# Optimization experiments

Measured on AMD Instinct MI355X. Metric: run time of the kernel, lower is better.

Reference implementation:

```python
import jax, jax.numpy as jnp
import numpy as np

D_IN = 1024
D_OUT = 1024
N_HEADS = 16
D_H = D_OUT // N_HEADS


def setup_inputs() -> dict:
    key = jax.random.key(0)
    k_x, k_q, k_k, k_v = jax.random.split(key, 4)
    x = jax.random.normal(k_x, (4, 2048, D_IN), dtype=jnp.float32)
    s = 1.0 / np.sqrt(D_IN)
    # weights stored as [d_in, d_out] (transpose of torch Linear.weight)
    W_q = jax.random.uniform(k_q, (D_IN, D_OUT), dtype=jnp.float32, minval=-s, maxval=s)
    W_k = jax.random.uniform(k_k, (D_IN, D_OUT), dtype=jnp.float32, minval=-s, maxval=s)
    W_v = jax.random.uniform(k_v, (D_IN, D_OUT), dtype=jnp.float32, minval=-s, maxval=s)
    return {"x": x, "W_q": W_q, "W_k": W_k, "W_v": W_v}


def reference(x, W_q, W_k, W_v):
    B, T, _ = x.shape
    # QKV projections -> [B, H, T, d_h]
    def split_heads(y):
        return y.reshape(B, T, N_HEADS, D_H).transpose(0, 2, 1, 3)
    q = split_heads(x @ W_q)
    k = split_heads(x @ W_k)
    v = split_heads(x @ W_v)
    # attention scores [B, H, T, T]
    scores = jnp.einsum('bhqd,bhkd->bhqk', q, k)
    causal = jnp.tril(jnp.ones((T, T), dtype=bool))  # True = keep
    scores = jnp.where(causal, scores, -jnp.inf)
    weights = jax.nn.softmax(scores / np.sqrt(D_H), axis=-1)
    ctx = jnp.einsum('bhqk,bhkd->bhqd', weights, v)  # [B,H,T,d_h]
    return ctx.transpose(0, 2, 1, 3).reshape(B, T, D_OUT)
```

## Files before the change

### kernel.cpp

```cpp
#include <hip/hip_runtime.h>
#include <stdint.h>

typedef float f32x4 __attribute__((ext_vector_type(4)));
typedef __bf16 bf16x8 __attribute__((ext_vector_type(8)));

#define LOG2E 1.4426950408889634f
#define SCL2 (0.125f * LOG2E)

static __device__ __forceinline__ unsigned short f2bf(float f) {
  unsigned int u = __builtin_bit_cast(unsigned int, f);
  u += 0x7fffu + ((u >> 16) & 1u);
  return (unsigned short)(u >> 16);
}

static __device__ __forceinline__ void gload16(const void* g, void* l) {
  __builtin_amdgcn_global_load_lds(
      (const __attribute__((address_space(1))) unsigned int*)g,
      (__attribute__((address_space(3))) unsigned int*)l, 16, 0, 0);
}

__global__ void cvt_x_kernel(const float* __restrict__ x, unsigned short* __restrict__ xb) {
  size_t i = ((size_t)blockIdx.x * 256 + threadIdx.x) * 8;
  const float4 a = *(const float4*)(x + i);
  const float4 b = *(const float4*)(x + i + 4);
  union { unsigned short us[8]; uint4 u; } o;
  o.us[0] = f2bf(a.x); o.us[1] = f2bf(a.y); o.us[2] = f2bf(a.z); o.us[3] = f2bf(a.w);
  o.us[4] = f2bf(b.x); o.us[5] = f2bf(b.y); o.us[6] = f2bf(b.z); o.us[7] = f2bf(b.w);
  *(uint4*)(xb + i) = o.u;
}

__global__ void wt_kernel(const float* __restrict__ Wq, const float* __restrict__ Wk,
                          const float* __restrict__ Wv, unsigned short* __restrict__ Wt) {
  __shared__ float t[32][33];
  const int z = blockIdx.z;
  const float* W = (z == 0) ? Wq : ((z == 1) ? Wk : Wv);
  unsigned short* o = Wt + (size_t)z * 1048576;
  const int k0 = blockIdx.y * 32, n0 = blockIdx.x * 32;
  const int tx = threadIdx.x, ty = threadIdx.y;
#pragma unroll
  for (int i = 0; i < 4; ++i)
    t[ty + i * 8][tx] = W[(size_t)(k0 + ty + i * 8) * 1024 + n0 + tx];
  __syncthreads();
#pragma unroll
  for (int i = 0; i < 4; ++i)
    o[(size_t)(n0 + ty + i * 8) * 1024 + k0 + tx] = f2bf(t[tx][ty + i * 8]);
}

__global__ __launch_bounds__(256) void gemm_qkv(
    const unsigned short* __restrict__ xb, const unsigned short* __restrict__ Wt,
    unsigned short* __restrict__ Qb, unsigned short* __restrict__ Kb,
    unsigned short* __restrict__ Vtb) {
  __shared__ uint4 ldsab[2048];
  char* ldsc = (char*)ldsab;
  const int tid = threadIdx.x;
  const int lane = tid & 63;
  const int li = lane & 15, g = lane >> 4;
  const int wv = tid >> 6, wr = wv >> 1, wc = wv & 1;
  const int L = blockIdx.x;
  const int W = (L & 7) * 192 + (L >> 3);
  const int z = W >> 9;
  const int rem = W & 511;
  const int m0 = (rem >> 3) * 128, n0 = (rem & 7) * 128;
  const char* Abase = (const char*)xb;
  const char* Bbase = (const char*)(Wt + (size_t)z * 1048576);

  const f32x4 fz = {0.f, 0.f, 0.f, 0.f};
  f32x4 acc[4][4];
#pragma unroll
  for (int m = 0; m < 4; ++m)
#pragma unroll
    for (int n = 0; n < 4; ++n) acc[m][n] = fz;

  for (int kt = 0; kt < 16; ++kt) {
    __syncthreads();
#pragma unroll
    for (int i = 0; i < 4; ++i) {
      const int c = i * 256 + tid, r = c >> 3, cr = c & 7;
      gload16(Abase + (size_t)(m0 + r) * 2048 + kt * 128 + ((cr ^ (r & 7)) * 16),
              ldsc + c * 16);
      gload16(Bbase + (size_t)(n0 + r) * 2048 + kt * 128 + ((cr ^ (r & 7)) * 16),
              ldsc + 16384 + c * 16);
    }
    __syncthreads();
#pragma unroll
    for (int ks = 0; ks < 2; ++ks) {
      bf16x8 a[4], b[4];
#pragma unroll
      for (int m = 0; m < 4; ++m) {
        const int ra = wr * 64 + m * 16 + li;
        a[m] = *(const bf16x8*)(ldsc + ra * 128 + (((ks * 4 + g) ^ (ra & 7)) * 16));
      }
#pragma unroll
      for (int n = 0; n < 4; ++n) {
        const int rb = wc * 64 + n * 16 + li;
        b[n] = *(const bf16x8*)(ldsc + 16384 + rb * 128 + (((ks * 4 + g) ^ (rb & 7)) * 16));
      }
#pragma unroll
      for (int m = 0; m < 4; ++m)
#pragma unroll
        for (int n = 0; n < 4; ++n)
          acc[m][n] = __builtin_amdgcn_mfma_f32_16x16x32_bf16(a[m], b[n], acc[m][n], 0, 0, 0);
    }
  }

  if (z == 2) {
    __syncthreads();
    char* tb = ldsc + wv * 8192;
#pragma unroll
    for (int m = 0; m < 4; ++m)
#pragma unroll
      for (int n = 0; n < 4; ++n) {
        const int d_l = n * 16 + li;
#pragma unroll
        for (int rp = 0; rp < 2; ++rp) {
          const int t_l = m * 16 + g * 4 + rp * 2;
          const unsigned lo = f2bf(acc[m][n][rp * 2]);
          const unsigned hi2 = f2bf(acc[m][n][rp * 2 + 1]);
          *(unsigned*)(tb + d_l * 128 + (((t_l >> 3) ^ (d_l & 7)) * 16) + (t_l & 7) * 2) =
              lo | (hi2 << 16);
        }
      }
    __syncthreads();
    const int t0g = m0 + wr * 64;
    const int bI2 = t0g >> 11, tt2 = t0g & 2047;
    const int hh = (n0 + wc * 64) >> 6;
#pragma unroll
    for (int p2 = 0; p2 < 8; ++p2) {
      const int d_l = p2 * 8 + (lane >> 3);
      const int c8 = lane & 7;
      const uint4 v = *(const uint4*)(tb + d_l * 128 + ((c8 ^ (d_l & 7)) * 16));
      *(uint4*)((char*)Vtb +
                ((((size_t)(bI2 * 16 + hh) * 64 + d_l) * 2048 + tt2 + c8 * 8) * 2)) = v;
    }
  } else {
    unsigned short* dst = (z == 0) ? Qb : Kb;
    const float sc = (z == 0) ? SCL2 : 1.0f;
#pragma unroll
    for (int m = 0; m < 4; ++m) {
#pragma unroll
      for (int r = 0; r < 4; ++r) {
        const int mg = m0 + wr * 64 + m * 16 + g * 4 + r;
        const int bI = mg >> 11, t = mg & 2047;
#pragma unroll
        for (int n = 0; n < 4; ++n) {
          const int ng = n0 + wc * 64 + n * 16 + li;
          const int h = ng >> 6, d = ng & 63;
          dst[((size_t)(bI * 16 + h) * 2048 + t) * 64 + d] = f2bf(acc[m][n][r] * sc);
        }
      }
    }
  }
}

__global__ __launch_bounds__(512, 4) void attn_kernel(
    const unsigned short* __restrict__ Qb, const unsigned short* __restrict__ Kb,
    const unsigned short* __restrict__ Vtb, float* __restrict__ out) {
  __shared__ uint4 lds[4096];
  char* ldsc = (char*)lds;
  const int L = blockIdx.x;
  const int W = (L & 7) * 64 + (L >> 3);
  const int bh = W >> 3;
  const int qp = W & 7;
  const int tid = threadIdx.x;
  const int lane = tid & 63, wv = tid >> 6;
  const int grp = wv >> 2, wq = wv & 3;
  const int t256 = tid & 255;
  const int li = lane & 15, g = lane >> 4;

  char* gbase = ldsc + grp * 32768;

  const char* Qrow = (const char*)Qb + (size_t)bh * 2048 * 128;
  const char* Krow = (const char*)Kb + (size_t)bh * 2048 * 128;
  const char* Vrow = (const char*)Vtb + (size_t)bh * 64 * 4096;
  const int bI = bh >> 4, h = bh & 15;
  const f32x4 fz = {0.f, 0.f, 0.f, 0.f};

  union { unsigned int u[4]; bf16x8 v; } onesu;
  onesu.u[0] = 0x3F803F80u; onesu.u[1] = 0x3F803F80u;
  onesu.u[2] = 0x3F803F80u; onesu.u[3] = 0x3F803F80u;
  const bf16x8 ones = onesu.v;

  auto stage = [&](int b, int kt) {
#pragma unroll
    for (int i = 0; i < 2; ++i) {
      const int c = i * 256 + t256, r = c >> 3, cr = c & 7;
      gload16(Krow + (size_t)(kt * 64 + r) * 128 + ((cr ^ (r & 7)) * 16),
              gbase + b * 16384 + c * 16);
      gload16(Vrow + (size_t)r * 4096 + kt * 128 + ((cr ^ (r & 7)) * 16),
              gbase + b * 16384 + 8192 + c * 16);
    }
  };

  for (int half = 0; half < 2; ++half) {
    const int qt = half ? (15 - qp) : qp;
    const int q0 = qt * 128;
    const int qw = q0 + wq * 32;
    const int hc = qt + 1;
    const int kbeg = grp ? hc : 0;

    uint4 qf[2][2];
#pragma unroll
    for (int nq = 0; nq < 2; ++nq)
#pragma unroll
      for (int ks = 0; ks < 2; ++ks)
        qf[nq][ks] = *(const uint4*)(Qrow + (size_t)(qw + nq * 16 + li) * 128 + ks * 64 + g * 16);

    float mrow[2] = {-1e30f, -1e30f};
    float lrow[2] = {0.0f, 0.0f};
    f32x4 lsum[2] = {fz, fz};
    f32x4 ctx[4][2];
#pragma unroll
    for (int mtd = 0; mtd < 4; ++mtd)
#pragma unroll
      for (int nq = 0; nq < 2; ++nq) ctx[mtd][nq] = fz;

    stage(0, kbeg);

    for (int it = 0; it < hc; ++it) {
      const int kt = kbeg + it;
      __syncthreads();
      if (it + 1 < hc) stage((it + 1) & 1, kt + 1);
      if (kt * 64 > qw + 31) continue;

      const char* sK = gbase + (it & 1) * 16384;
      const char* sV = sK + 8192;

      f32x4 st[4][2];
#pragma unroll
      for (int mt = 0; mt < 4; ++mt)
#pragma unroll
        for (int nq = 0; nq < 2; ++nq) st[mt][nq] = fz;
      __builtin_amdgcn_s_setprio(1);
#pragma unroll
      for (int ks = 0; ks < 2; ++ks) {
        bf16x8 kf[4];
#pragma unroll
        for (int mt = 0; mt < 4; ++mt) {
          const int rk = mt * 16 + li;
          kf[mt] = *(const bf16x8*)(sK + rk * 128 + (((ks * 4 + g) ^ (rk & 7)) * 16));
        }
#pragma unroll
        for (int mt = 0; mt < 4; ++mt)
#pragma unroll
          for (int nq = 0; nq < 2; ++nq)
            st[mt][nq] = __builtin_amdgcn_mfma_f32_16x16x32_bf16(
                kf[mt], __builtin_bit_cast(bf16x8, qf[nq][ks]), st[mt][nq], 0, 0, 0);
      }
      __builtin_amdgcn_s_setprio(0);

      const bool full = (kt * 64 + 63 <= qw);
      bf16x8 pb[2][2];
#pragma unroll
      for (int nq = 0; nq < 2; ++nq) {
        float p[4][4];
        if (full) {
#pragma unroll
          for (int mt = 0; mt < 4; ++mt)
#pragma unroll
            for (int r = 0; r < 4; ++r) p[mt][r] = st[mt][nq][r];
        } else {
          const int qg_ = qw + nq * 16 + li;
#pragma unroll
          for (int mt = 0; mt < 4; ++mt)
#pragma unroll
            for (int r = 0; r < 4; ++r)
              p[mt][r] = (kt * 64 + mt * 16 + g * 4 + r > qg_) ? -__builtin_inff()
                                                               : st[mt][nq][r];
        }
        const float m1 = fmaxf(fmaxf(p[0][0], p[0][1]), p[0][2]);
        const float m2 = fmaxf(fmaxf(p[0][3], p[1][0]), p[1][1]);
        const float m3 = fmaxf(fmaxf(p[1][2], p[1][3]), p[2][0]);
        const float m4 = fmaxf(fmaxf(p[2][1], p[2][2]), p[2][3]);
        const float m5 = fmaxf(fmaxf(p[3][0], p[3][1]), p[3][2]);
        const float lmax = fmaxf(fmaxf(fmaxf(m1, m2), m3), fmaxf(fmaxf(m4, m5), p[3][3]));
        if (!__all(lmax <= mrow[nq] + 8.0f)) {
          float tmax = fmaxf(lmax, __shfl_xor(lmax, 16, 64));
          tmax = fmaxf(tmax, __shfl_xor(tmax, 32, 64));
          const float mnew = fmaxf(mrow[nq], tmax);
          const float resc = __builtin_amdgcn_exp2f(mrow[nq] - mnew);
          mrow[nq] = mnew;
          lsum[nq] = lsum[nq] * resc;
#pragma unroll
          for (int mtd = 0; mtd < 4; ++mtd) ctx[mtd][nq] = ctx[mtd][nq] * resc;
        }
        const float mcur = mrow[nq];
#pragma unroll
        for (int mt = 0; mt < 4; ++mt)
#pragma unroll
          for (int r = 0; r < 4; ++r)
            p[mt][r] = __builtin_amdgcn_exp2f(p[mt][r] - mcur);
#pragma unroll
        for (int ks2 = 0; ks2 < 2; ++ks2) {
          union { __bf16 b[8]; bf16x8 v; } u;
#pragma unroll
          for (int r = 0; r < 4; ++r) {
            u.b[r] = (__bf16)p[2 * ks2][r];
            u.b[4 + r] = (__bf16)p[2 * ks2 + 1][r];
          }
          pb[nq][ks2] = u.v;
        }
      }

      __builtin_amdgcn_s_setprio(1);
#pragma unroll
      for (int ks2 = 0; ks2 < 2; ++ks2) {
#pragma unroll
        for (int mtd = 0; mtd < 4; ++mtd) {
          const int rd = mtd * 16 + li;
          const char* vb = sV + rd * 128;
          const uint2 lo = *(const uint2*)(vb + (((ks2 * 4 + (g >> 1)) ^ (rd & 7)) * 16) + (g & 1) * 8);
          const uint2 hi = *(const uint2*)(vb + (((ks2 * 4 + 2 + (g >> 1)) ^ (rd & 7)) * 16) + (g & 1) * 8);
          uint4 vv; vv.x = lo.x; vv.y = lo.y; vv.z = hi.x; vv.w = hi.y;
          const bf16x8 vf = __builtin_bit_cast(bf16x8, vv);
#pragma unroll
          for (int nq = 0; nq < 2; ++nq)
            ctx[mtd][nq] = __builtin_amdgcn_mfma_f32_16x16x32_bf16(vf, pb[nq][ks2], ctx[mtd][nq], 0, 0, 0);
        }
#pragma unroll
        for (int nq = 0; nq < 2; ++nq)
          lsum[nq] = __builtin_amdgcn_mfma_f32_16x16x32_bf16(ones, pb[nq][ks2], lsum[nq], 0, 0, 0);
      }
      __builtin_amdgcn_s_setprio(0);
    }

    lrow[0] = lsum[0][0];
    lrow[1] = lsum[1][0];

    __syncthreads();
    if (grp == 1) {
      char* mb = ldsc + 32768;
#pragma unroll
      for (int nqp = 0; nqp < 2; ++nqp)
#pragma unroll
        for (int mtd = 0; mtd < 4; ++mtd)
          *(f32x4*)(mb + (wq * 64 + lane) * 128 + nqp * 64 + ((mtd ^ (lane & 3)) * 16)) = ctx[mtd][nqp];
      if (g == 0) {
#pragma unroll
        for (int nqp = 0; nqp < 2; ++nqp) {
          ((float*)ldsc)[nqp * 64 + wq * 16 + li] = mrow[nqp];
          ((float*)(ldsc + 512))[nqp * 64 + wq * 16 + li] = lrow[nqp];
        }
      }
    }
    __syncthreads();
    if (grp == 0) {
      const char* mb = ldsc + 32768;
#pragma unroll
      for (int nqp = 0; nqp < 2; ++nqp) {
        const float mB = ((const float*)ldsc)[nqp * 64 + wq * 16 + li];
        const float lB = ((const float*)(ldsc + 512))[nqp * 64 + wq * 16 + li];
        const float mM = fmaxf(mrow[nqp], mB);
        const float cA = __builtin_amdgcn_exp2f(mrow[nqp] - mM);
        const float cB = __builtin_amdgcn_exp2f(mB - mM);
        const float inv = 1.0f / (lrow[nqp] * cA + lB * cB);
        const float fA = cA * inv, fB = cB * inv;
#pragma unroll
        for (int mtd = 0; mtd < 4; ++mtd) {
          const f32x4 cb = *(const f32x4*)(mb + (wq * 64 + lane) * 128 + nqp * 64 + ((mtd ^ (lane & 3)) * 16));
          ctx[mtd][nqp] = ctx[mtd][nqp] * fA + cb * fB;
        }
      }
    }
    __syncthreads();

    if (grp == 0) {
      float* trb = (float*)(ldsc + wq * 8192);
#pragma unroll
      for (int nqp = 0; nqp < 2; ++nqp)
#pragma unroll
        for (int mtd = 0; mtd < 4; ++mtd)
#pragma unroll
          for (int r = 0; r < 4; ++r) {
            const int q = nqp * 16 + li;
            const int d = mtd * 16 + g * 4 + r;
            trb[q * 64 + ((((d >> 2) ^ (q & 15)) << 2) | (d & 3))] = ctx[mtd][nqp][r];
          }
    }
    __syncthreads();
    if (grp == 0) {
      const float* trb = (const float*)(ldsc + wq * 8192);
#pragma unroll
      for (int pass = 0; pass < 8; ++pass) {
        const int qr = pass * 4 + g;
        const float4 v = *(const float4*)&trb[qr * 64 + ((li ^ (qr & 15)) << 2)];
        *(float4*)(out + ((size_t)bI * 2048 + q0 + wq * 32 + qr) * 1024 + h * 64 + li * 4) = v;
      }
    }
    __syncthreads();
  }
}

extern "C" void kernel_launch(void* const* d_in, const int* in_sizes, int n_in,
                              void* d_out, int out_size, void* d_ws, size_t ws_size,
                              hipStream_t stream) {
  (void)in_sizes; (void)n_in; (void)out_size; (void)ws_size;
  const float* x  = (const float*)d_in[0];
  const float* Wq = (const float*)d_in[1];
  const float* Wk = (const float*)d_in[2];
  const float* Wv = (const float*)d_in[3];
  float* out = (float*)d_out;
  char* ws = (char*)d_ws;
  unsigned short* xb  = (unsigned short*)ws;
  unsigned short* Wt  = (unsigned short*)(ws + 16777216);
  unsigned short* Qb  = (unsigned short*)(ws + 23068672);
  unsigned short* Kb  = (unsigned short*)(ws + 39845888);
  unsigned short* Vtb = (unsigned short*)(ws + 56623104);

  hipLaunchKernelGGL(cvt_x_kernel, dim3(4096), dim3(256), 0, stream, x, xb);
  hipLaunchKernelGGL(wt_kernel, dim3(32, 32, 3), dim3(32, 8), 0, stream, Wq, Wk, Wv, Wt);
  hipLaunchKernelGGL(gemm_qkv, dim3(1536), dim3(256), 0, stream, xb, Wt, Qb, Kb, Vtb);
  hipLaunchKernelGGL(attn_kernel, dim3(512), dim3(512), 0, stream, Qb, Kb, Vtb, out);
}
```

Measured before the change: 178.5 us.

## Merge prep kernels, stage Q/K stores through LDS, permute V layout for single loads

Fuses the x-to-bf16 conversion and weight transpose into one launch, which removes one kernel launch. Q and K outputs are now staged through swizzled LDS and written as coalesced 16-byte stores instead of scattered 2-byte stores. V^T is written with a permuted element order so the attention kernel can fetch each MFMA operand with one 16-byte LDS read instead of two 8-byte reads and a repack. The cost is an extra LDS round-trip and barrier in the GEMM epilogue, and correctness depends on the V permutation matching the P operand order.

```diff
diff --git a/kernel.cpp b/kernel.cpp
--- a/kernel.cpp
+++ b/kernel.cpp
@@ -19,31 +19,34 @@
       (__attribute__((address_space(3))) unsigned int*)l, 16, 0, 0);
 }
 
-__global__ void cvt_x_kernel(const float* __restrict__ x, unsigned short* __restrict__ xb) {
-  size_t i = ((size_t)blockIdx.x * 256 + threadIdx.x) * 8;
-  const float4 a = *(const float4*)(x + i);
-  const float4 b = *(const float4*)(x + i + 4);
-  union { unsigned short us[8]; uint4 u; } o;
-  o.us[0] = f2bf(a.x); o.us[1] = f2bf(a.y); o.us[2] = f2bf(a.z); o.us[3] = f2bf(a.w);
-  o.us[4] = f2bf(b.x); o.us[5] = f2bf(b.y); o.us[6] = f2bf(b.z); o.us[7] = f2bf(b.w);
-  *(uint4*)(xb + i) = o.u;
-}
-
-__global__ void wt_kernel(const float* __restrict__ Wq, const float* __restrict__ Wk,
-                          const float* __restrict__ Wv, unsigned short* __restrict__ Wt) {
+__global__ void prep_kernel(const float* __restrict__ x, const float* __restrict__ Wq,
+                            const float* __restrict__ Wk, const float* __restrict__ Wv,
+                            unsigned short* __restrict__ xb, unsigned short* __restrict__ Wt) {
   __shared__ float t[32][33];
-  const int z = blockIdx.z;
-  const float* W = (z == 0) ? Wq : ((z == 1) ? Wk : Wv);
-  unsigned short* o = Wt + (size_t)z * 1048576;
-  const int k0 = blockIdx.y * 32, n0 = blockIdx.x * 32;
-  const int tx = threadIdx.x, ty = threadIdx.y;
-#pragma unroll
-  for (int i = 0; i < 4; ++i)
-    t[ty + i * 8][tx] = W[(size_t)(k0 + ty + i * 8) * 1024 + n0 + tx];
-  __syncthreads();
-#pragma unroll
-  for (int i = 0; i < 4; ++i)
-    o[(size_t)(n0 + ty + i * 8) * 1024 + k0 + tx] = f2bf(t[tx][ty + i * 8]);
+  if (blockIdx.x < 4096) {
+    size_t i = ((size_t)blockIdx.x * 256 + threadIdx.x) * 8;
+    const float4 a = *(const float4*)(x + i);
+    const float4 b = *(const float4*)(x + i + 4);
+    union { unsigned short us[8]; uint4 u; } o;
+    o.us[0] = f2bf(a.x); o.us[1] = f2bf(a.y); o.us[2] = f2bf(a.z); o.us[3] = f2bf(a.w);
+    o.us[4] = f2bf(b.x); o.us[5] = f2bf(b.y); o.us[6] = f2bf(b.z); o.us[7] = f2bf(b.w);
+    *(uint4*)(xb + i) = o.u;
+  } else {
+    const int b = blockIdx.x - 4096;
+    const int z = b >> 10;
+    const int rem = b & 1023;
+    const float* W = (z == 0) ? Wq : ((z == 1) ? Wk : Wv);
+    unsigned short* o = Wt + (size_t)z * 1048576;
+    const int k0 = (rem >> 5) * 32, n0 = (rem & 31) * 32;
+    const int tx = threadIdx.x & 31, ty = threadIdx.x >> 5;
+#pragma unroll
+    for (int i = 0; i < 4; ++i)
+      t[ty + i * 8][tx] = W[(size_t)(k0 + ty + i * 8) * 1024 + n0 + tx];
+    __syncthreads();
+#pragma unroll
+    for (int i = 0; i < 4; ++i)
+      o[(size_t)(n0 + ty + i * 8) * 1024 + k0 + tx] = f2bf(t[tx][ty + i * 8]);
+  }
 }
 
 __global__ __launch_bounds__(256) void gemm_qkv(
@@ -103,9 +106,9 @@
     }
   }
 
+  __syncthreads();
+  char* tb = ldsc + wv * 8192;
   if (z == 2) {
-    __syncthreads();
-    char* tb = ldsc + wv * 8192;
 #pragma unroll
     for (int m = 0; m < 4; ++m)
 #pragma unroll
@@ -114,9 +117,14 @@
 #pragma unroll
         for (int rp = 0; rp < 2; ++rp) {
           const int t_l = m * 16 + g * 4 + rp * 2;
+          const int t5 = t_l & 31;
+          const int ks2 = t_l >> 5;
+          const int rr = t5 & 15;
+          const int gp = ((rr >> 3) & 1) * 2 + ((rr >> 2) & 1);
+          const int j = (t5 & 3) + ((t5 >> 4) << 2);
           const unsigned lo = f2bf(acc[m][n][rp * 2]);
           const unsigned hi2 = f2bf(acc[m][n][rp * 2 + 1]);
-          *(unsigned*)(tb + d_l * 128 + (((t_l >> 3) ^ (d_l & 7)) * 16) + (t_l & 7) * 2) =
+          *(unsigned*)(tb + d_l * 128 + (((ks2 * 4 + gp) ^ (d_l & 7)) * 16) + j * 2) =
               lo | (hi2 << 16);
         }
       }
@@ -133,21 +141,31 @@
                 ((((size_t)(bI2 * 16 + hh) * 64 + d_l) * 2048 + tt2 + c8 * 8) * 2)) = v;
     }
   } else {
-    unsigned short* dst = (z == 0) ? Qb : Kb;
     const float sc = (z == 0) ? SCL2 : 1.0f;
 #pragma unroll
-    for (int m = 0; m < 4; ++m) {
-#pragma unroll
-      for (int r = 0; r < 4; ++r) {
-        const int mg = m0 + wr * 64 + m * 16 + g * 4 + r;
-        const int bI = mg >> 11, t = mg & 2047;
-#pragma unroll
-        for (int n = 0; n < 4; ++n) {
-          const int ng = n0 + wc * 64 + n * 16 + li;
-          const int h = ng >> 6, d = ng & 63;
-          dst[((size_t)(bI * 16 + h) * 2048 + t) * 64 + d] = f2bf(acc[m][n][r] * sc);
-        }
-      }
+    for (int m = 0; m < 4; ++m)
+#pragma unroll
+      for (int n = 0; n < 4; ++n) {
+        const int ch = n * 2 + (li >> 3);
+        const int eo = (li & 7) * 2;
+#pragma unroll
+        for (int r = 0; r < 4; ++r) {
+          const int t_l = m * 16 + g * 4 + r;
+          *(unsigned short*)(tb + t_l * 128 + ((ch ^ (t_l & 7)) * 16) + eo) =
+              f2bf(acc[m][n][r] * sc);
+        }
+      }
+    __syncthreads();
+    const int t0g = m0 + wr * 64;
+    const int bI = t0g >> 11, tt = t0g & 2047;
+    const int h = (n0 + wc * 64) >> 6;
+    unsigned short* dst = ((z == 0) ? Qb : Kb) + ((size_t)(bI * 16 + h) * 2048 + tt) * 64;
+#pragma unroll
+    for (int p = 0; p < 8; ++p) {
+      const int t_l = p * 8 + (lane >> 3);
+      const int c8 = lane & 7;
+      const uint4 v = *(const uint4*)(tb + t_l * 128 + ((c8 ^ (t_l & 7)) * 16));
+      *(uint4*)((char*)dst + t_l * 128 + c8 * 16) = v;
     }
   }
 }
@@ -307,11 +325,8 @@
 #pragma unroll
         for (int mtd = 0; mtd < 4; ++mtd) {
           const int rd = mtd * 16 + li;
-          const char* vb = sV + rd * 128;
-          const uint2 lo = *(const uint2*)(vb + (((ks2 * 4 + (g >> 1)) ^ (rd & 7)) * 16) + (g & 1) * 8);
-          const uint2 hi = *(const uint2*)(vb + (((ks2 * 4 + 2 + (g >> 1)) ^ (rd & 7)) * 16) + (g & 1) * 8);
-          uint4 vv; vv.x = lo.x; vv.y = lo.y; vv.z = hi.x; vv.w = hi.y;
-          const bf16x8 vf = __builtin_bit_cast(bf16x8, vv);
+          const bf16x8 vf =
+              *(const bf16x8*)(sV + rd * 128 + (((ks2 * 4 + g) ^ (rd & 7)) * 16));
 #pragma unroll
           for (int nq = 0; nq < 2; ++nq)
             ctx[mtd][nq] = __builtin_amdgcn_mfma_f32_16x16x32_bf16(vf, pb[nq][ks2], ctx[mtd][nq], 0, 0, 0);
@@ -406,8 +421,8 @@
   unsigned short* Kb  = (unsigned short*)(ws + 39845888);
   unsigned short* Vtb = (unsigned short*)(ws + 56623104);
 
-  hipLaunchKernelGGL(cvt_x_kernel, dim3(4096), dim3(256), 0, stream, x, xb);
-  hipLaunchKernelGGL(wt_kernel, dim3(32, 32, 3), dim3(32, 8), 0, stream, Wq, Wk, Wv, Wt);
+  hipLaunchKernelGGL(prep_kernel, dim3(4096 + 3072), dim3(256), 0, stream,
+                     x, Wq, Wk, Wv, xb, Wt);
   hipLaunchKernelGGL(gemm_qkv, dim3(1536), dim3(256), 0, stream, xb, Wt, Qb, Kb, Vtb);
   hipLaunchKernelGGL(attn_kernel, dim3(512), dim3(512), 0, stream, Qb, Kb, Vtb, out);
 }
```

Measured after the change: 165.1 us (median of 5 runs). -7.5%, faster.
